# Performance work log

Measured on AMD Instinct MI355X. Metric: run time of the kernel, lower is better.

## Reference

```python
import jax, jax.numpy as jnp
import numpy as np

N_USERS = 20000
N_ENTITIES = 80000
N = N_USERS + N_ENTITIES
EMBED_DIM = 128
CONV = [128, 128, 64, 32]  # [embed_dim] + eval(conv_dim_list)
NNZ = 1_600_000
CF_B = 8192
CF_L2_LAMBDA = 1e-5


def setup_inputs() -> dict:
    key = jax.random.key(0)
    ks = jax.random.split(key, 20)
    inp = {}
    inp["embed_table"] = jax.random.normal(ks[0], (N, EMBED_DIM), jnp.float32) * 0.02
    ki = 1
    for l in range(3):
        din, dout = CONV[l], CONV[l + 1]
        s = 1.0 / np.sqrt(din).astype(np.float32)
        inp[f"W1_{l}"] = jax.random.normal(ks[ki], (din, dout), jnp.float32) * s; ki += 1
        inp[f"b1_{l}"] = jnp.zeros((dout,), jnp.float32)
        inp[f"W2_{l}"] = jax.random.normal(ks[ki], (din, dout), jnp.float32) * s; ki += 1
        inp[f"b2_{l}"] = jnp.zeros((dout,), jnp.float32)
    inp["edge_rows"] = jax.random.randint(ks[7], (NNZ,), 0, N, jnp.int32)
    inp["edge_cols"] = jax.random.randint(ks[8], (NNZ,), 0, N, jnp.int32)
    # Laplacian-like normalized attention values (positive, ~1/degree scale)
    inp["edge_vals"] = jax.random.uniform(ks[9], (NNZ,), jnp.float32) / 16.0
    inp["user_ids"] = jax.random.randint(ks[10], (CF_B,), 0, N_USERS, jnp.int32)
    inp["item_pos_ids"] = jax.random.randint(ks[11], (CF_B,), N_USERS, N, jnp.int32)
    inp["item_neg_ids"] = jax.random.randint(ks[12], (CF_B,), N_USERS, N, jnp.int32)
    return inp


def _l2_normalize(x):
    # F.normalize(x, p=2, dim=1): x / max(||x||_2, eps)
    n = jnp.linalg.norm(x, axis=1, keepdims=True)
    return x / jnp.maximum(n, 1e-12)


def _l2_loss_mean(x):
    return jnp.mean(jnp.sum(x * x, axis=1) / 2.0)


def _calc_cf_embeddings(embed_table, layer_params, edge_rows, edge_cols, edge_vals):
    n = embed_table.shape[0]
    ego = embed_table
    outs = [ego]
    for (W1, b1, W2, b2) in layer_params:
        # sparse A @ ego via gather + segment_sum (SpMM in COO form)
        msgs = edge_vals[:, None] * ego[edge_cols]          # [nnz, d_in]
        side = jax.ops.segment_sum(msgs, edge_rows, num_segments=n)  # [n, d_in]
        # bi-interaction aggregator (mess_dropout = 0)
        ego = (jax.nn.leaky_relu((ego + side) @ W1 + b1)
               + jax.nn.leaky_relu((ego * side) @ W2 + b2))
        outs.append(_l2_normalize(ego))
    return jnp.concatenate(outs, axis=1)  # [n, 128+128+64+32]


def reference(embed_table, W1_0, b1_0, W2_0, b2_0, W1_1, b1_1, W2_1, b2_1,
              W1_2, b1_2, W2_2, b2_2, edge_rows, edge_cols, edge_vals,
              user_ids, item_pos_ids, item_neg_ids):
    layer_params = [(W1_0, b1_0, W2_0, b2_0),
                    (W1_1, b1_1, W2_1, b2_1),
                    (W1_2, b1_2, W2_2, b2_2)]
    all_embed = _calc_cf_embeddings(embed_table, layer_params,
                                    edge_rows, edge_cols, edge_vals)
    u = all_embed[user_ids]
    p = all_embed[item_pos_ids]
    ng = all_embed[item_neg_ids]
    pos_score = jnp.sum(u * p, axis=1)
    neg_score = jnp.sum(u * ng, axis=1)
    cf_loss = jnp.mean(-jax.nn.log_sigmoid(pos_score - neg_score))
    l2 = _l2_loss_mean(u) + _l2_loss_mean(p) + _l2_loss_mean(ng)
    return cf_loss + CF_L2_LAMBDA * l2
```

## Files before the change

kernel.cpp:

```cpp
#include <hip/hip_runtime.h>
#include <math.h>

static constexpr int N_NODES = 100000;
static constexpr int NNZ     = 1600000;
static constexpr int CFB     = 8192;
static constexpr int NBUCK   = (N_NODES + 63) / 64;
static constexpr int N4      = N_NODES * 128 / 4;
static constexpr int NCHUNK  = 512;
static constexpr int EPC     = NNZ / NCHUNK;
static constexpr int NE      = NBUCK * NCHUNK;

static constexpr int WOF_10 = 0;
static constexpr int WOF_20 = 16384;
static constexpr int WOF_11 = 32768;
static constexpr int WOF_21 = 40960;
static constexpr int WOF_12 = 49152;
static constexpr int WOF_22 = 51200;
static constexpr int WTOT   = 53248;

typedef short bf16x8 __attribute__((ext_vector_type(8)));
typedef float f32x4  __attribute__((ext_vector_type(4)));
typedef float f32x2  __attribute__((ext_vector_type(2)));

__device__ __forceinline__ float lrelu(float x) { return x >= 0.0f ? x : 0.01f * x; }

__device__ __forceinline__ unsigned short f2bf(float x) {
  unsigned u = __float_as_uint(x);
  u += 0x7FFFu + ((u >> 16) & 1u);
  return (unsigned short)(u >> 16);
}
__device__ __forceinline__ float bf2f(unsigned short h) {
  return __uint_as_float(((unsigned)h) << 16);
}
__device__ __forceinline__ unsigned pack2(float x, float y) {
  return (unsigned)f2bf(x) | ((unsigned)f2bf(y) << 16);
}

__global__ __launch_bounds__(256)
void cvt_kernel(const float* __restrict__ in, unsigned short* __restrict__ out_bf,
                unsigned char* __restrict__ out_q) {
  int i = blockIdx.x * 256 + threadIdx.x;
  if (i < N4) {
    float4 v = reinterpret_cast<const float4*>(in)[i];
    uint2 o; o.x = pack2(v.x, v.y); o.y = pack2(v.z, v.w);
    reinterpret_cast<uint2*>(out_bf)[i] = o;
    int q = __builtin_amdgcn_cvt_pk_fp8_f32(v.x * 1024.f, v.y * 1024.f, 0, false);
    q = __builtin_amdgcn_cvt_pk_fp8_f32(v.z * 1024.f, v.w * 1024.f, q, true);
    reinterpret_cast<unsigned*>(out_q)[i] = (unsigned)q;
  }
}

__global__ __launch_bounds__(256)
void wprep_kernel(const float* __restrict__ W1_0, const float* __restrict__ W2_0,
                  const float* __restrict__ W1_1, const float* __restrict__ W2_1,
                  const float* __restrict__ W1_2, const float* __restrict__ W2_2,
                  unsigned short* __restrict__ wt) {
  int i = blockIdx.x * 256 + threadIdx.x;
  if (i >= WTOT) return;
  const float* src; int off, din, dout;
  if      (i < WOF_20) { src = W1_0; off = WOF_10; din = 128; dout = 128; }
  else if (i < WOF_11) { src = W2_0; off = WOF_20; din = 128; dout = 128; }
  else if (i < WOF_21) { src = W1_1; off = WOF_11; din = 128; dout = 64;  }
  else if (i < WOF_12) { src = W2_1; off = WOF_21; din = 128; dout = 64;  }
  else if (i < WOF_22) { src = W1_2; off = WOF_12; din = 64;  dout = 32;  }
  else                 { src = W2_2; off = WOF_22; din = 64;  dout = 32;  }
  int j = i - off;
  int c = j / din;
  int k = j % din;
  wt[i] = f2bf(src[(size_t)k * dout + c]);
}

__global__ __launch_bounds__(256)
void binhist(const int* __restrict__ erows, int* __restrict__ cnt) {
  __shared__ int h[NBUCK];
  for (int b = threadIdx.x; b < NBUCK; b += 256) h[b] = 0;
  __syncthreads();
  const int c = blockIdx.x;
  const int e0 = c * EPC, e1 = e0 + EPC;
  for (int i = e0 + threadIdx.x; i < e1; i += 256)
    atomicAdd(&h[erows[i] >> 6], 1);
  __syncthreads();
  for (int b = threadIdx.x; b < NBUCK; b += 256)
    cnt[c * NBUCK + b] = h[b];
}

__global__ __launch_bounds__(512)
void bucket_scan(int* __restrict__ cnt, int* __restrict__ btot) {
  __shared__ int s[NCHUNK];
  const int b = blockIdx.x;
  const int t = threadIdx.x;
  int v = cnt[(size_t)t * NBUCK + b];
  s[t] = v;
  __syncthreads();
  for (int off = 1; off < NCHUNK; off <<= 1) {
    int x = (t >= off) ? s[t - off] : 0;
    __syncthreads();
    s[t] += x;
    __syncthreads();
  }
  cnt[(size_t)t * NBUCK + b] = s[t] - v;
  if (t == NCHUNK - 1) btot[b] = s[t];
}

__global__ __launch_bounds__(256)
void base_scan(const int* __restrict__ btot, int* __restrict__ bbase) {
  __shared__ int tsum[256];
  const int t = threadIdx.x;
  int loc[8];
  int s = 0;
  #pragma unroll
  for (int j = 0; j < 8; ++j) {
    int idx = t * 8 + j;
    int v = (idx < NBUCK) ? btot[idx] : 0;
    loc[j] = s; s += v;
  }
  tsum[t] = s;
  __syncthreads();
  for (int off = 1; off < 256; off <<= 1) {
    int v = (t >= off) ? tsum[t - off] : 0;
    __syncthreads();
    tsum[t] += v;
    __syncthreads();
  }
  int base = (t == 0) ? 0 : tsum[t - 1];
  #pragma unroll
  for (int j = 0; j < 8; ++j) {
    int idx = t * 8 + j;
    if (idx < NBUCK) bbase[idx] = base + loc[j];
  }
  if (t == 0) bbase[NBUCK] = NNZ;
}

__global__ __launch_bounds__(256)
void scatter_bucket(const int* __restrict__ erows, const int* __restrict__ ecols,
                    const float* __restrict__ evals, const int* __restrict__ cnt,
                    const int* __restrict__ bbase, uint2* __restrict__ spackA) {
  __shared__ int cur[NBUCK];
  const int c = blockIdx.x;
  for (int b = threadIdx.x; b < NBUCK; b += 256)
    cur[b] = bbase[b] + cnt[c * NBUCK + b];
  __syncthreads();
  const int e0 = c * EPC, e1 = e0 + EPC;
  for (int i = e0 + threadIdx.x; i < e1; i += 256) {
    int r = erows[i];
    int p = atomicAdd(&cur[r >> 6], 1);
    uint2 rec;
    rec.x = (unsigned)ecols[i] | ((unsigned)(r & 63) << 17);
    rec.y = __float_as_uint(evals[i]);
    spackA[p] = rec;
  }
}

__global__ __launch_bounds__(256)
void bucket_sort(const int* __restrict__ bbase, const uint2* __restrict__ spackA,
                 uint2* __restrict__ spackB, int* __restrict__ row_ptr) {
  __shared__ int hist[64];
  __shared__ int hcur[64];
  const int b = blockIdx.x;
  const int tid = threadIdx.x;
  const int j0 = bbase[b], j1 = bbase[b + 1];
  if (tid < 64) hist[tid] = 0;
  __syncthreads();
  for (int k = j0 + tid; k < j1; k += 256)
    atomicAdd(&hist[(spackA[k].x >> 17) & 63], 1);
  __syncthreads();
  if (tid == 0) {
    int s = 0, row0 = b * 64;
    for (int r = 0; r < 64; ++r) {
      int v = hist[r];
      hcur[r] = s;
      if (row0 + r < N_NODES) row_ptr[row0 + r] = j0 + s;
      s += v;
    }
    if (b == NBUCK - 1) row_ptr[N_NODES] = NNZ;
  }
  __syncthreads();
  for (int k = j0 + tid; k < j1; k += 256) {
    uint2 rec = spackA[k];
    int rl = (rec.x >> 17) & 63;
    int p = j0 + atomicAdd(&hcur[rl], 1);
    spackB[p] = rec;
  }
}

template<int DIN>
__global__ __launch_bounds__(256)
void spmm_fp8(const unsigned char* __restrict__ qtab, float inv_scale,
              const int* __restrict__ row_ptr,
              const uint2* __restrict__ spack,
              unsigned short* __restrict__ side) {
  int row  = blockIdx.x * 4 + (threadIdx.x >> 6);
  int lane = threadIdx.x & 63;
  if (row >= N_NODES) return;
  int j0 = row_ptr[row], j1 = row_ptr[row + 1];
  if constexpr (DIN == 128) {
    float ax = 0.f, ay = 0.f;
    #pragma unroll 8
    for (int j = j0; j < j1; ++j) {
      uint2 rec = spack[j];
      float v = __uint_as_float(rec.y);
      unsigned q = *reinterpret_cast<const unsigned short*>(
          qtab + (size_t)(rec.x & 0x1FFFF) * 128 + lane * 2);
      f32x2 xy = __builtin_amdgcn_cvt_pk_f32_fp8(q, false);
      ax += v * xy.x;  ay += v * xy.y;
    }
    *reinterpret_cast<unsigned*>(side + (size_t)row * 128 + lane * 2) =
        pack2(ax * inv_scale, ay * inv_scale);
  } else {
    float a = 0.f;
    #pragma unroll 8
    for (int j = j0; j < j1; ++j) {
      uint2 rec = spack[j];
      unsigned q = qtab[(size_t)(rec.x & 0x1FFFF) * DIN + lane];
      a += __uint_as_float(rec.y) * __builtin_amdgcn_cvt_f32_fp8(q, 0);
    }
    side[(size_t)row * DIN + lane] = f2bf(a * inv_scale);
  }
}

template<int DIN, int DOUT, int WM, int WN, int TPB, bool QOUT>
__global__ __launch_bounds__(256)
void bi_mfma(const unsigned short* __restrict__ ego,
             const unsigned short* __restrict__ side,
             const unsigned short* __restrict__ W1t, const float* __restrict__ b1,
             const unsigned short* __restrict__ W2t, const float* __restrict__ b2,
             unsigned short* __restrict__ out,
             unsigned char* __restrict__ outq, float qs) {
  static_assert(WM * WN == 4, "4 waves");
  constexpr int KFRAG = DIN / 32;
  constexpr int NCOLS = DOUT / WN;
  constexpr int NFRAG = NCOLS / 16;
  constexpr int MROWS = 32 / WM;
  constexpr int MFRAG = MROWS / 16;
  constexpr int CPR   = DIN / 8;
  constexpr int CHUNKS = 32 * CPR;

  __shared__ __align__(16) unsigned short lds1[32 * DIN];
  __shared__ __align__(16) unsigned short lds2[32 * DIN];

  const int tid  = threadIdx.x;
  const int wid  = tid >> 6;
  const int lane = tid & 63;
  const int n0   = (wid % WN) * NCOLS;
  const int mrow0 = (wid / WN) * MROWS;
  const int lr   = lane & 15;
  const int lk   = (lane >> 4) * 8;

  bf16x8 w1f[KFRAG][NFRAG], w2f[KFRAG][NFRAG];
  #pragma unroll
  for (int kf = 0; kf < KFRAG; ++kf)
    #pragma unroll
    for (int nf = 0; nf < NFRAG; ++nf) {
      int col = n0 + nf * 16 + lr;
      int kr  = kf * 32 + lk;
      w1f[kf][nf] = *reinterpret_cast<const bf16x8*>(W1t + (size_t)col * DIN + kr);
      w2f[kf][nf] = *reinterpret_cast<const bf16x8*>(W2t + (size_t)col * DIN + kr);
    }
  float b1v[NFRAG], b2v[NFRAG];
  #pragma unroll
  for (int nf = 0; nf < NFRAG; ++nf) {
    b1v[nf] = b1[n0 + nf * 16 + lr];
    b2v[nf] = b2[n0 + nf * 16 + lr];
  }

  for (int t = 0; t < TPB; ++t) {
    int row0 = (blockIdx.x * TPB + t) * 32;
    if (row0 >= N_NODES) break;
    __syncthreads();
    for (int ci = tid; ci < CHUNKS; ci += 256) {
      int r  = ci / CPR;
      int c8 = ci % CPR;
      size_t g = (size_t)(row0 + r) * DIN + c8 * 8;
      uint4 e4 = *reinterpret_cast<const uint4*>(ego + g);
      uint4 s4 = *reinterpret_cast<const uint4*>(side + g);
      uint4 h1v, h2v;
      {
        float ex, ey, sx, sy;
        ex = bf2f((unsigned short)(e4.x & 0xFFFFu)); ey = bf2f((unsigned short)(e4.x >> 16));
        sx = bf2f((unsigned short)(s4.x & 0xFFFFu)); sy = bf2f((unsigned short)(s4.x >> 16));
        h1v.x = pack2(ex + sx, ey + sy); h2v.x = pack2(ex * sx, ey * sy);
        ex = bf2f((unsigned short)(e4.y & 0xFFFFu)); ey = bf2f((unsigned short)(e4.y >> 16));
        sx = bf2f((unsigned short)(s4.y & 0xFFFFu)); sy = bf2f((unsigned short)(s4.y >> 16));
        h1v.y = pack2(ex + sx, ey + sy); h2v.y = pack2(ex * sx, ey * sy);
        ex = bf2f((unsigned short)(e4.z & 0xFFFFu)); ey = bf2f((unsigned short)(e4.z >> 16));
        sx = bf2f((unsigned short)(s4.z & 0xFFFFu)); sy = bf2f((unsigned short)(s4.z >> 16));
        h1v.z = pack2(ex + sx, ey + sy); h2v.z = pack2(ex * sx, ey * sy);
        ex = bf2f((unsigned short)(e4.w & 0xFFFFu)); ey = bf2f((unsigned short)(e4.w >> 16));
        sx = bf2f((unsigned short)(s4.w & 0xFFFFu)); sy = bf2f((unsigned short)(s4.w >> 16));
        h1v.w = pack2(ex + sx, ey + sy); h2v.w = pack2(ex * sx, ey * sy);
      }
      unsigned byte = ((unsigned)(r * DIN + c8 * 8)) * 2u;
      byte ^= (unsigned)((r & 7) << 4);
      *reinterpret_cast<uint4*>(reinterpret_cast<char*>(lds1) + byte) = h1v;
      *reinterpret_cast<uint4*>(reinterpret_cast<char*>(lds2) + byte) = h2v;
    }
    __syncthreads();

    f32x4 acc1[MFRAG][NFRAG], acc2[MFRAG][NFRAG];
    #pragma unroll
    for (int mf = 0; mf < MFRAG; ++mf)
      #pragma unroll
      for (int nf = 0; nf < NFRAG; ++nf) {
        acc1[mf][nf] = (f32x4)0.f;
        acc2[mf][nf] = (f32x4)0.f;
      }
    #pragma unroll
    for (int kf = 0; kf < KFRAG; ++kf) {
      bf16x8 a1[MFRAG], a2[MFRAG];
      #pragma unroll
      for (int mf = 0; mf < MFRAG; ++mf) {
        int r = mrow0 + mf * 16 + lr;
        unsigned byte = ((unsigned)(r * DIN + kf * 32 + lk)) * 2u;
        byte ^= (unsigned)((r & 7) << 4);
        a1[mf] = *reinterpret_cast<const bf16x8*>(reinterpret_cast<const char*>(lds1) + byte);
        a2[mf] = *reinterpret_cast<const bf16x8*>(reinterpret_cast<const char*>(lds2) + byte);
      }
      #pragma unroll
      for (int mf = 0; mf < MFRAG; ++mf)
        #pragma unroll
        for (int nf = 0; nf < NFRAG; ++nf) {
          acc1[mf][nf] = __builtin_amdgcn_mfma_f32_16x16x32_bf16(a1[mf], w1f[kf][nf], acc1[mf][nf], 0, 0, 0);
          acc2[mf][nf] = __builtin_amdgcn_mfma_f32_16x16x32_bf16(a2[mf], w2f[kf][nf], acc2[mf][nf], 0, 0, 0);
        }
    }

    #pragma unroll
    for (int mf = 0; mf < MFRAG; ++mf)
      #pragma unroll
      for (int nf = 0; nf < NFRAG; ++nf) {
        #pragma unroll
        for (int reg = 0; reg < 4; ++reg) {
          int r = row0 + mrow0 + mf * 16 + (lane >> 4) * 4 + reg;
          int c = n0 + nf * 16 + lr;
          float o = lrelu(acc1[mf][nf][reg] + b1v[nf]) + lrelu(acc2[mf][nf][reg] + b2v[nf]);
          out[(size_t)r * DOUT + c] = f2bf(o);
          if constexpr (QOUT) {
            float oq = o * qs;
            outq[(size_t)r * DOUT + c] =
                (unsigned char)(__builtin_amdgcn_cvt_pk_fp8_f32(oq, oq, 0, false) & 0xFF);
          }
        }
      }
  }
}

__global__ __launch_bounds__(256)
void score_all(const float* __restrict__ emb0,
               const unsigned short* __restrict__ e1,
               const unsigned short* __restrict__ e2,
               const unsigned short* __restrict__ e3,
               const int* __restrict__ uid, const int* __restrict__ pid,
               const int* __restrict__ nid,
               float* __restrict__ pos, float* __restrict__ neg,
               float* __restrict__ l2) {
  int i = blockIdx.x * 4 + (threadIdx.x >> 6);
  int lane = threadIdx.x & 63;
  if (i >= CFB) return;
  const int ui = uid[i], pi = pid[i], gi = nid[i];
  float PS = 0.f, NS = 0.f, L2 = 0.f;

  {
    float up = 0, un = 0, uu = 0, pp = 0, nn = 0;
    for (int d = lane; d < 128; d += 64) {
      float a = emb0[(size_t)ui * 128 + d];
      float b = emb0[(size_t)pi * 128 + d];
      float c = emb0[(size_t)gi * 128 + d];
      up += a * b; un += a * c; uu += a * a; pp += b * b; nn += c * c;
    }
    #pragma unroll
    for (int off = 32; off > 0; off >>= 1) {
      up += __shfl_xor(up, off); un += __shfl_xor(un, off);
      uu += __shfl_xor(uu, off); pp += __shfl_xor(pp, off); nn += __shfl_xor(nn, off);
    }
    PS += up; NS += un; L2 += uu + pp + nn;
  }
  const unsigned short* tabs[3] = { e1, e2, e3 };
  const int dims[3] = { 128, 64, 32 };
  #pragma unroll
  for (int L = 0; L < 3; ++L) {
    const unsigned short* T = tabs[L];
    const int dim = dims[L];
    float up = 0, un = 0, uu = 0, pp = 0, nn = 0;
    for (int d = lane; d < dim; d += 64) {
      float a = bf2f(T[(size_t)ui * dim + d]);
      float b = bf2f(T[(size_t)pi * dim + d]);
      float c = bf2f(T[(size_t)gi * dim + d]);
      up += a * b; un += a * c; uu += a * a; pp += b * b; nn += c * c;
    }
    #pragma unroll
    for (int off = 32; off > 0; off >>= 1) {
      up += __shfl_xor(up, off); un += __shfl_xor(un, off);
      uu += __shfl_xor(uu, off); pp += __shfl_xor(pp, off); nn += __shfl_xor(nn, off);
    }
    float mu = fmaxf(sqrtf(uu), 1e-12f);
    float mp = fmaxf(sqrtf(pp), 1e-12f);
    float mn = fmaxf(sqrtf(nn), 1e-12f);
    PS += up / (mu * mp);
    NS += un / (mu * mn);
    L2 += uu / (mu * mu) + pp / (mp * mp) + nn / (mn * mn);
  }
  if (lane == 0) { pos[i] = PS; neg[i] = NS; l2[i] = L2; }
}

__global__ __launch_bounds__(256)
void loss_kernel(const float* __restrict__ pos, const float* __restrict__ neg,
                 const float* __restrict__ l2, float* __restrict__ out) {
  __shared__ float s1[256];
  __shared__ float s2[256];
  int tid = threadIdx.x;
  float cf = 0.f, reg = 0.f;
  for (int i = tid; i < CFB; i += 256) {
    float x = pos[i] - neg[i];
    float sp = (x > 0.f) ? log1pf(expf(-x)) : (-x + log1pf(expf(x)));
    cf  += sp;
    reg += l2[i];
  }
  s1[tid] = cf; s2[tid] = reg;
  __syncthreads();
  for (int s = 128; s > 0; s >>= 1) {
    if (tid < s) { s1[tid] += s1[tid + s]; s2[tid] += s2[tid + s]; }
    __syncthreads();
  }
  if (tid == 0)
    out[0] = s1[0] / (float)CFB + 1e-5f * (0.5f * s2[0] / (float)CFB);
}

extern "C" void kernel_launch(void* const* d_in, const int* in_sizes, int n_in,
                              void* d_out, int out_size, void* d_ws, size_t ws_size,
                              hipStream_t stream) {
  const float* embed = (const float*)d_in[0];
  const float* W1_0 = (const float*)d_in[1];
  const float* b1_0 = (const float*)d_in[2];
  const float* W2_0 = (const float*)d_in[3];
  const float* b2_0 = (const float*)d_in[4];
  const float* W1_1 = (const float*)d_in[5];
  const float* b1_1 = (const float*)d_in[6];
  const float* W2_1 = (const float*)d_in[7];
  const float* b2_1 = (const float*)d_in[8];
  const float* W1_2 = (const float*)d_in[9];
  const float* b1_2 = (const float*)d_in[10];
  const float* W2_2 = (const float*)d_in[11];
  const float* b2_2 = (const float*)d_in[12];
  const int*   erows = (const int*)d_in[13];
  const int*   ecols = (const int*)d_in[14];
  const float* evals = (const float*)d_in[15];
  const int*   uid = (const int*)d_in[16];
  const int*   pid = (const int*)d_in[17];
  const int*   nid = (const int*)d_in[18];

  unsigned short* e0 = (unsigned short*)d_ws;
  unsigned short* e1 = e0 + (size_t)N_NODES * 128;
  unsigned short* e2 = e1 + (size_t)N_NODES * 128;
  unsigned short* e3 = e2 + (size_t)N_NODES * 64;
  unsigned short* sb = e3 + (size_t)N_NODES * 32;
  unsigned char*  q0 = (unsigned char*)(sb + (size_t)N_NODES * 128);
  unsigned char*  q2 = q0 + (size_t)N_NODES * 128;
  unsigned short* wt = (unsigned short*)(q2 + (size_t)N_NODES * 64);
  int*   cnt     = (int*)(wt + WTOT);
  int*   btot    = cnt + NE;
  int*   bbase   = btot + NBUCK;
  int*   row_ptr = bbase + NBUCK + 1;
  uint2* spackA  = (uint2*)(row_ptr + N_NODES + 2);
  uint2* spackB  = spackA + NNZ;
  unsigned char* q1 = (unsigned char*)spackA;
  float* posb    = (float*)(spackB + NNZ);
  float* negb    = posb + CFB;
  float* l2b     = negb + CFB;

  cvt_kernel<<<(N4 + 255) / 256, 256, 0, stream>>>(embed, e0, q0);
  wprep_kernel<<<(WTOT + 255) / 256, 256, 0, stream>>>(W1_0, W2_0, W1_1, W2_1, W1_2, W2_2, wt);
  binhist<<<NCHUNK, 256, 0, stream>>>(erows, cnt);
  bucket_scan<<<NBUCK, NCHUNK, 0, stream>>>(cnt, btot);
  base_scan<<<1, 256, 0, stream>>>(btot, bbase);
  scatter_bucket<<<NCHUNK, 256, 0, stream>>>(erows, ecols, evals, cnt, bbase, spackA);
  bucket_sort<<<NBUCK, 256, 0, stream>>>(bbase, spackA, spackB, row_ptr);

  constexpr int TPB = 5;
  constexpr int GB  = (N_NODES / 32 + TPB - 1) / TPB;

  spmm_fp8<128><<<(N_NODES + 3) / 4, 256, 0, stream>>>(q0, 1.f / 1024.f, row_ptr, spackB, sb);
  bi_mfma<128, 128, 1, 4, TPB, true><<<GB, 256, 0, stream>>>(e0, sb, wt + WOF_10, b1_0, wt + WOF_20, b2_0, e1, q1, 64.f);

  spmm_fp8<128><<<(N_NODES + 3) / 4, 256, 0, stream>>>(q1, 1.f / 64.f, row_ptr, spackB, sb);
  bi_mfma<128, 64, 1, 4, TPB, true><<<GB, 256, 0, stream>>>(e1, sb, wt + WOF_11, b1_1, wt + WOF_21, b2_1, e2, q2, 64.f);

  spmm_fp8<64><<<(N_NODES + 3) / 4, 256, 0, stream>>>(q2, 1.f / 64.f, row_ptr, spackB, sb);
  bi_mfma<64, 32, 2, 2, TPB, false><<<GB, 256, 0, stream>>>(e2, sb, wt + WOF_12, b1_2, wt + WOF_22, b2_2, e3, (unsigned char*)nullptr, 0.f);

  score_all<<<CFB / 4, 256, 0, stream>>>(embed, e1, e2, e3, uid, pid, nid, posb, negb, l2b);
  loss_kernel<<<1, 256, 0, stream>>>(posb, negb, l2b, (float*)d_out);
}
```

Before: 382.2 us.

## Fuse convert, weight prep and histogram kernels; sort edges within rows by column

Merges the embedding fp8/bf16 conversion, weight transpose and bucket histogram into one grid-stride kernel, removing two launches. The per-bucket sort now keys on both local row and high bits of the column index (8192-bin histogram with block scan), so edges inside each row come out roughly ordered by column. This is meant to improve gather locality in the SpMM passes. In exchange, bucket_sort uses much more shared memory and runs a longer scan.

```diff
diff --git a/kernel.cpp b/kernel.cpp
--- a/kernel.cpp
+++ b/kernel.cpp
@@ -37,51 +37,47 @@
 }
 
 __global__ __launch_bounds__(256)
-void cvt_kernel(const float* __restrict__ in, unsigned short* __restrict__ out_bf,
-                unsigned char* __restrict__ out_q) {
-  int i = blockIdx.x * 256 + threadIdx.x;
-  if (i < N4) {
-    float4 v = reinterpret_cast<const float4*>(in)[i];
+void cvt_fused(const float* __restrict__ embed, unsigned short* __restrict__ e0,
+               unsigned char* __restrict__ q0,
+               const float* __restrict__ W1_0, const float* __restrict__ W2_0,
+               const float* __restrict__ W1_1, const float* __restrict__ W2_1,
+               const float* __restrict__ W1_2, const float* __restrict__ W2_2,
+               unsigned short* __restrict__ wt,
+               const int* __restrict__ erows, int* __restrict__ cnt) {
+  __shared__ int h[NBUCK];
+  for (int b = threadIdx.x; b < NBUCK; b += 256) h[b] = 0;
+  __syncthreads();
+  const int c = blockIdx.x;
+  const int e0i = c * EPC, e1i = e0i + EPC;
+  for (int i = e0i + threadIdx.x; i < e1i; i += 256)
+    atomicAdd(&h[erows[i] >> 6], 1);
+  __syncthreads();
+  for (int b = threadIdx.x; b < NBUCK; b += 256)
+    cnt[c * NBUCK + b] = h[b];
+
+  const int gid    = blockIdx.x * 256 + threadIdx.x;
+  const int stride = NCHUNK * 256;
+  for (int i = gid; i < N4; i += stride) {
+    float4 v = reinterpret_cast<const float4*>(embed)[i];
     uint2 o; o.x = pack2(v.x, v.y); o.y = pack2(v.z, v.w);
-    reinterpret_cast<uint2*>(out_bf)[i] = o;
+    reinterpret_cast<uint2*>(e0)[i] = o;
     int q = __builtin_amdgcn_cvt_pk_fp8_f32(v.x * 1024.f, v.y * 1024.f, 0, false);
     q = __builtin_amdgcn_cvt_pk_fp8_f32(v.z * 1024.f, v.w * 1024.f, q, true);
-    reinterpret_cast<unsigned*>(out_q)[i] = (unsigned)q;
-  }
-}
-
-__global__ __launch_bounds__(256)
-void wprep_kernel(const float* __restrict__ W1_0, const float* __restrict__ W2_0,
-                  const float* __restrict__ W1_1, const float* __restrict__ W2_1,
-                  const float* __restrict__ W1_2, const float* __restrict__ W2_2,
-                  unsigned short* __restrict__ wt) {
-  int i = blockIdx.x * 256 + threadIdx.x;
-  if (i >= WTOT) return;
-  const float* src; int off, din, dout;
-  if      (i < WOF_20) { src = W1_0; off = WOF_10; din = 128; dout = 128; }
-  else if (i < WOF_11) { src = W2_0; off = WOF_20; din = 128; dout = 128; }
-  else if (i < WOF_21) { src = W1_1; off = WOF_11; din = 128; dout = 64;  }
-  else if (i < WOF_12) { src = W2_1; off = WOF_21; din = 128; dout = 64;  }
-  else if (i < WOF_22) { src = W1_2; off = WOF_12; din = 64;  dout = 32;  }
-  else                 { src = W2_2; off = WOF_22; din = 64;  dout = 32;  }
-  int j = i - off;
-  int c = j / din;
-  int k = j % din;
-  wt[i] = f2bf(src[(size_t)k * dout + c]);
-}
-
-__global__ __launch_bounds__(256)
-void binhist(const int* __restrict__ erows, int* __restrict__ cnt) {
-  __shared__ int h[NBUCK];
-  for (int b = threadIdx.x; b < NBUCK; b += 256) h[b] = 0;
-  __syncthreads();
-  const int c = blockIdx.x;
-  const int e0 = c * EPC, e1 = e0 + EPC;
-  for (int i = e0 + threadIdx.x; i < e1; i += 256)
-    atomicAdd(&h[erows[i] >> 6], 1);
-  __syncthreads();
-  for (int b = threadIdx.x; b < NBUCK; b += 256)
-    cnt[c * NBUCK + b] = h[b];
+    reinterpret_cast<unsigned*>(q0)[i] = (unsigned)q;
+  }
+  for (int i = gid; i < WTOT; i += stride) {
+    const float* src; int off, din, dout;
+    if      (i < WOF_20) { src = W1_0; off = WOF_10; din = 128; dout = 128; }
+    else if (i < WOF_11) { src = W2_0; off = WOF_20; din = 128; dout = 128; }
+    else if (i < WOF_21) { src = W1_1; off = WOF_11; din = 128; dout = 64;  }
+    else if (i < WOF_12) { src = W2_1; off = WOF_21; din = 128; dout = 64;  }
+    else if (i < WOF_22) { src = W1_2; off = WOF_12; din = 64;  dout = 32;  }
+    else                 { src = W2_2; off = WOF_22; din = 64;  dout = 32;  }
+    int j = i - off;
+    int cc = j / din;
+    int k  = j % din;
+    wt[i] = f2bf(src[(size_t)k * dout + cc]);
+  }
 }
 
 __global__ __launch_bounds__(512)
@@ -154,31 +150,50 @@
 __global__ __launch_bounds__(256)
 void bucket_sort(const int* __restrict__ bbase, const uint2* __restrict__ spackA,
                  uint2* __restrict__ spackB, int* __restrict__ row_ptr) {
-  __shared__ int hist[64];
-  __shared__ int hcur[64];
+  __shared__ int hist[8192];
+  __shared__ int tsum[256];
   const int b = blockIdx.x;
-  const int tid = threadIdx.x;
+  const int t = threadIdx.x;
   const int j0 = bbase[b], j1 = bbase[b + 1];
-  if (tid < 64) hist[tid] = 0;
-  __syncthreads();
-  for (int k = j0 + tid; k < j1; k += 256)
-    atomicAdd(&hist[(spackA[k].x >> 17) & 63], 1);
-  __syncthreads();
-  if (tid == 0) {
-    int s = 0, row0 = b * 64;
-    for (int r = 0; r < 64; ++r) {
-      int v = hist[r];
-      hcur[r] = s;
-      if (row0 + r < N_NODES) row_ptr[row0 + r] = j0 + s;
-      s += v;
-    }
-    if (b == NBUCK - 1) row_ptr[N_NODES] = NNZ;
-  }
-  __syncthreads();
-  for (int k = j0 + tid; k < j1; k += 256) {
+  #pragma unroll
+  for (int j = 0; j < 32; ++j) hist[t * 32 + j] = 0;
+  __syncthreads();
+  for (int k = j0 + t; k < j1; k += 256) {
+    unsigned x = spackA[k].x;
+    int key = (int)(((x >> 17) & 63) << 7) | (int)((x & 0x1FFFF) >> 10);
+    atomicAdd(&hist[key], 1);
+  }
+  __syncthreads();
+  int s = 0;
+  #pragma unroll
+  for (int j = 0; j < 32; ++j) s += hist[t * 32 + j];
+  tsum[t] = s;
+  __syncthreads();
+  for (int off = 1; off < 256; off <<= 1) {
+    int v = (t >= off) ? tsum[t - off] : 0;
+    __syncthreads();
+    tsum[t] += v;
+    __syncthreads();
+  }
+  int run = tsum[t] - s;
+  #pragma unroll
+  for (int j = 0; j < 32; ++j) {
+    int v = hist[t * 32 + j];
+    hist[t * 32 + j] = run;
+    run += v;
+  }
+  __syncthreads();
+  if (t < 64) {
+    int row = b * 64 + t;
+    if (row < N_NODES) row_ptr[row] = j0 + hist[t * 128];
+  }
+  if (b == NBUCK - 1 && t == 0) row_ptr[N_NODES] = NNZ;
+  __syncthreads();
+  for (int k = j0 + t; k < j1; k += 256) {
     uint2 rec = spackA[k];
-    int rl = (rec.x >> 17) & 63;
-    int p = j0 + atomicAdd(&hcur[rl], 1);
+    unsigned x = rec.x;
+    int key = (int)(((x >> 17) & 63) << 7) | (int)((x & 0x1FFFF) >> 10);
+    int p = j0 + atomicAdd(&hist[key], 1);
     spackB[p] = rec;
   }
 }
@@ -467,9 +482,8 @@
   float* negb    = posb + CFB;
   float* l2b     = negb + CFB;
 
-  cvt_kernel<<<(N4 + 255) / 256, 256, 0, stream>>>(embed, e0, q0);
-  wprep_kernel<<<(WTOT + 255) / 256, 256, 0, stream>>>(W1_0, W2_0, W1_1, W2_1, W1_2, W2_2, wt);
-  binhist<<<NCHUNK, 256, 0, stream>>>(erows, cnt);
+  cvt_fused<<<NCHUNK, 256, 0, stream>>>(embed, e0, q0, W1_0, W2_0, W1_1, W2_1,
+                                        W1_2, W2_2, wt, erows, cnt);
   bucket_scan<<<NBUCK, NCHUNK, 0, stream>>>(cnt, btot);
   base_scan<<<1, 256, 0, stream>>>(btot, bbase);
   scatter_bucket<<<NCHUNK, 256, 0, stream>>>(erows, ecols, evals, cnt, bbase, spackA);
```

Result: slower. 391.2 us (+2.3%).

## Fuse embedding conversion, weight prep and bucket histogram; split-edge SpMM for dim 64

Applied to the files above, without the earlier changes.

Merges the embedding bf16/fp8 conversion, the weight transpose-to-bf16 and the per-chunk row histogram into one grid-strided kernel, which removes two launches. The 64-wide SpMM path now has each half-wave take alternate edges and load two fp8 values per lane, then combines the halves with a shuffle. This is meant to halve the serial edge loop per row and widen each gather. In exchange, the fused kernel runs only 512 blocks for the conversion, so bandwidth could suffer from lower parallelism.

```diff
diff --git a/kernel.cpp b/kernel.cpp
--- a/kernel.cpp
+++ b/kernel.cpp
@@ -37,51 +37,47 @@
 }
 
 __global__ __launch_bounds__(256)
-void cvt_kernel(const float* __restrict__ in, unsigned short* __restrict__ out_bf,
-                unsigned char* __restrict__ out_q) {
-  int i = blockIdx.x * 256 + threadIdx.x;
-  if (i < N4) {
-    float4 v = reinterpret_cast<const float4*>(in)[i];
+void cvt_fused(const float* __restrict__ embed, unsigned short* __restrict__ e0,
+               unsigned char* __restrict__ q0,
+               const float* __restrict__ W1_0, const float* __restrict__ W2_0,
+               const float* __restrict__ W1_1, const float* __restrict__ W2_1,
+               const float* __restrict__ W1_2, const float* __restrict__ W2_2,
+               unsigned short* __restrict__ wt,
+               const int* __restrict__ erows, int* __restrict__ cnt) {
+  __shared__ int h[NBUCK];
+  for (int b = threadIdx.x; b < NBUCK; b += 256) h[b] = 0;
+  __syncthreads();
+  const int c = blockIdx.x;
+  const int e0i = c * EPC, e1i = e0i + EPC;
+  for (int i = e0i + threadIdx.x; i < e1i; i += 256)
+    atomicAdd(&h[erows[i] >> 6], 1);
+  __syncthreads();
+  for (int b = threadIdx.x; b < NBUCK; b += 256)
+    cnt[c * NBUCK + b] = h[b];
+
+  const int gid    = blockIdx.x * 256 + threadIdx.x;
+  const int stride = NCHUNK * 256;
+  for (int i = gid; i < N4; i += stride) {
+    float4 v = reinterpret_cast<const float4*>(embed)[i];
     uint2 o; o.x = pack2(v.x, v.y); o.y = pack2(v.z, v.w);
-    reinterpret_cast<uint2*>(out_bf)[i] = o;
+    reinterpret_cast<uint2*>(e0)[i] = o;
     int q = __builtin_amdgcn_cvt_pk_fp8_f32(v.x * 1024.f, v.y * 1024.f, 0, false);
     q = __builtin_amdgcn_cvt_pk_fp8_f32(v.z * 1024.f, v.w * 1024.f, q, true);
-    reinterpret_cast<unsigned*>(out_q)[i] = (unsigned)q;
-  }
-}
-
-__global__ __launch_bounds__(256)
-void wprep_kernel(const float* __restrict__ W1_0, const float* __restrict__ W2_0,
-                  const float* __restrict__ W1_1, const float* __restrict__ W2_1,
-                  const float* __restrict__ W1_2, const float* __restrict__ W2_2,
-                  unsigned short* __restrict__ wt) {
-  int i = blockIdx.x * 256 + threadIdx.x;
-  if (i >= WTOT) return;
-  const float* src; int off, din, dout;
-  if      (i < WOF_20) { src = W1_0; off = WOF_10; din = 128; dout = 128; }
-  else if (i < WOF_11) { src = W2_0; off = WOF_20; din = 128; dout = 128; }
-  else if (i < WOF_21) { src = W1_1; off = WOF_11; din = 128; dout = 64;  }
-  else if (i < WOF_12) { src = W2_1; off = WOF_21; din = 128; dout = 64;  }
-  else if (i < WOF_22) { src = W1_2; off = WOF_12; din = 64;  dout = 32;  }
-  else                 { src = W2_2; off = WOF_22; din = 64;  dout = 32;  }
-  int j = i - off;
-  int c = j / din;
-  int k = j % din;
-  wt[i] = f2bf(src[(size_t)k * dout + c]);
-}
-
-__global__ __launch_bounds__(256)
-void binhist(const int* __restrict__ erows, int* __restrict__ cnt) {
-  __shared__ int h[NBUCK];
-  for (int b = threadIdx.x; b < NBUCK; b += 256) h[b] = 0;
-  __syncthreads();
-  const int c = blockIdx.x;
-  const int e0 = c * EPC, e1 = e0 + EPC;
-  for (int i = e0 + threadIdx.x; i < e1; i += 256)
-    atomicAdd(&h[erows[i] >> 6], 1);
-  __syncthreads();
-  for (int b = threadIdx.x; b < NBUCK; b += 256)
-    cnt[c * NBUCK + b] = h[b];
+    reinterpret_cast<unsigned*>(q0)[i] = (unsigned)q;
+  }
+  for (int i = gid; i < WTOT; i += stride) {
+    const float* src; int off, din, dout;
+    if      (i < WOF_20) { src = W1_0; off = WOF_10; din = 128; dout = 128; }
+    else if (i < WOF_11) { src = W2_0; off = WOF_20; din = 128; dout = 128; }
+    else if (i < WOF_21) { src = W1_1; off = WOF_11; din = 128; dout = 64;  }
+    else if (i < WOF_12) { src = W2_1; off = WOF_21; din = 128; dout = 64;  }
+    else if (i < WOF_22) { src = W1_2; off = WOF_12; din = 64;  dout = 32;  }
+    else                 { src = W2_2; off = WOF_22; din = 64;  dout = 32;  }
+    int j = i - off;
+    int cc = j / din;
+    int k  = j % din;
+    wt[i] = f2bf(src[(size_t)k * dout + cc]);
+  }
 }
 
 __global__ __launch_bounds__(512)
@@ -207,14 +203,23 @@
     *reinterpret_cast<unsigned*>(side + (size_t)row * 128 + lane * 2) =
         pack2(ax * inv_scale, ay * inv_scale);
   } else {
-    float a = 0.f;
+    const int half = lane >> 5;
+    const int hl   = lane & 31;
+    float ax = 0.f, ay = 0.f;
     #pragma unroll 8
-    for (int j = j0; j < j1; ++j) {
+    for (int j = j0 + half; j < j1; j += 2) {
       uint2 rec = spack[j];
-      unsigned q = qtab[(size_t)(rec.x & 0x1FFFF) * DIN + lane];
-      a += __uint_as_float(rec.y) * __builtin_amdgcn_cvt_f32_fp8(q, 0);
-    }
-    side[(size_t)row * DIN + lane] = f2bf(a * inv_scale);
+      float v = __uint_as_float(rec.y);
+      unsigned q = *reinterpret_cast<const unsigned short*>(
+          qtab + (size_t)(rec.x & 0x1FFFF) * 64 + hl * 2);
+      f32x2 xy = __builtin_amdgcn_cvt_pk_f32_fp8(q, false);
+      ax += v * xy.x;  ay += v * xy.y;
+    }
+    ax += __shfl_xor(ax, 32);
+    ay += __shfl_xor(ay, 32);
+    if (lane < 32)
+      *reinterpret_cast<unsigned*>(side + (size_t)row * 64 + hl * 2) =
+          pack2(ax * inv_scale, ay * inv_scale);
   }
 }
 
@@ -467,9 +472,8 @@
   float* negb    = posb + CFB;
   float* l2b     = negb + CFB;
 
-  cvt_kernel<<<(N4 + 255) / 256, 256, 0, stream>>>(embed, e0, q0);
-  wprep_kernel<<<(WTOT + 255) / 256, 256, 0, stream>>>(W1_0, W2_0, W1_1, W2_1, W1_2, W2_2, wt);
-  binhist<<<NCHUNK, 256, 0, stream>>>(erows, cnt);
+  cvt_fused<<<NCHUNK, 256, 0, stream>>>(embed, e0, q0, W1_0, W2_0, W1_1, W2_1,
+                                        W1_2, W2_2, wt, erows, cnt);
   bucket_scan<<<NBUCK, NCHUNK, 0, stream>>>(cnt, btot);
   base_scan<<<1, 256, 0, stream>>>(btot, bbase);
   scatter_bucket<<<NCHUNK, 256, 0, stream>>>(erows, ecols, evals, cnt, bbase, spackA);
```

New measurement: 376.2 us (median of 2 runs). About the same (-1.6%).
